# Kernel optimization log

Hardware: AMD Instinct MI355X
Metric: run time of the kernel (lower is better)

The kernel has to match this reference:

```python
import jax, jax.numpy as jnp
import numpy as np

N = 100000
E = 1600000
D_IN = 256
HID = 128
EPS = 1e-5


def setup_inputs() -> dict:
    key = jax.random.key(0)
    ks = jax.random.split(key, 8)
    x = jax.random.normal(ks[0], (N, D_IN), dtype=jnp.float32)
    edge_index = jax.random.randint(ks[1], (2, E), 0, N, dtype=jnp.int64)
    edge_weight = jax.random.uniform(ks[2], (E,), dtype=jnp.float32)
    # GCNConv lin weights (glorot-ish scale) + bias
    W1 = jax.random.normal(ks[3], (D_IN, HID), dtype=jnp.float32) / np.sqrt(D_IN)
    b1 = jnp.zeros((HID,), dtype=jnp.float32)
    W2 = jax.random.normal(ks[4], (HID, HID), dtype=jnp.float32) / np.sqrt(HID)
    b2 = jnp.zeros((HID,), dtype=jnp.float32)
    # BatchNorm affine params
    g1 = jnp.ones((HID,), dtype=jnp.float32)
    be1 = jnp.zeros((HID,), dtype=jnp.float32)
    g2 = jnp.ones((HID,), dtype=jnp.float32)
    be2 = jnp.zeros((HID,), dtype=jnp.float32)
    return {"x": x, "edge_index": edge_index, "edge_weight": edge_weight,
            "W1": W1, "b1": b1, "g1": g1, "be1": be1,
            "W2": W2, "b2": b2, "g2": g2, "be2": be2}


def _gcn_layer(h, src, dst, w, W, b):
    # GCNConv(add_self_loops=False, normalize=False):
    # h' = h @ W; out[i] = sum_{(j->i)} w_ji * h'[j]; out += b
    h = h @ W                                   # [N, out_dim]
    msg = w[:, None] * jnp.take(h, src, axis=0)  # [E, out_dim]
    agg = jax.ops.segment_sum(msg, dst, num_segments=N)
    return agg + b


def _bn(h, gamma, beta):
    # BatchNorm1d with batch statistics (biased variance), training-mode math
    mean = jnp.mean(h, axis=0)
    var = jnp.mean(jnp.square(h - mean), axis=0)
    return (h - mean) * jax.lax.rsqrt(var + EPS) * gamma + beta


def reference(x, edge_index, edge_weight, W1, b1, g1, be1, W2, b2, g2, be2):
    src = edge_index[0]
    dst = edge_index[1]
    h = _gcn_layer(x, src, dst, edge_weight, W1, b1)
    h = jax.nn.relu(_bn(h, g1, be1))
    h = _gcn_layer(h, src, dst, edge_weight, W2, b2)
    h = jax.nn.relu(_bn(h, g2, be2))  # last_activation=True
    return h
```

## Files before the change

kernel.cpp:

```cpp
#include <hip/hip_runtime.h>
#include <hip/hip_bf16.h>

#define NNODES 100000
#define DIN    256
#define NHID   128
#define EPS    1e-5f
#define SHIFT  9
#define NB2    ((NNODES + 511) >> SHIFT)
#define BCAP2  9216
#define CURPAD 16
#define PH     2048

typedef __attribute__((ext_vector_type(8))) short short8v;
typedef __attribute__((ext_vector_type(4))) float f32x4;

static __device__ __forceinline__ unsigned short f2bf(float v) {
    __hip_bfloat16 b = __float2bfloat16(v);
    return *reinterpret_cast<unsigned short*>(&b);
}
static __device__ __forceinline__ float bfhi2f(unsigned int u) {
    union { unsigned int i; float f; } x; x.i = u & 0xFFFF0000u; return x.f;
}
static __device__ __forceinline__ float bflo2f(unsigned int u) {
    union { unsigned int i; float f; } x; x.i = u << 16; return x.f;
}

__global__ __launch_bounds__(256) void wtrans2_kernel(const float* __restrict__ W1,
                                                      const float* __restrict__ W2,
                                                      unsigned short* __restrict__ Wt1,
                                                      unsigned short* __restrict__ Wt2) {
    int i = blockIdx.x * 256 + threadIdx.x;
    if (i < DIN * NHID) {
        const int k = i >> 7, c = i & 127;
        Wt1[c * DIN + k] = f2bf(W1[i]);
    } else {
        i -= DIN * NHID;
        if (i < NHID * NHID) {
            const int k = i >> 7, c = i & 127;
            Wt2[c * NHID + k] = f2bf(W2[i]);
        }
    }
}

template <int K, int MODE>
__global__ __launch_bounds__(256) void mfma_gemm(const float* __restrict__ Af,
                                                 const unsigned short* __restrict__ Wtb,
                                                 const float* __restrict__ SS,
                                                 unsigned short* __restrict__ C, int M) {
    __shared__ float ssl[256];
    const int t = threadIdx.x;
    if (MODE == 1) {
        if (t < 256) ssl[t] = SS[t];
        __syncthreads();
    }

    const int wid = t >> 6;
    const int lane = t & 63;
    const int wr = wid >> 1, wc = wid & 1;
    const int l15 = lane & 15, g = lane >> 4;
    const int R0 = blockIdx.x * 128 + wr * 64;

    f32x4 acc[4][4] = {};

    for (int s = 0; s < K / 32; ++s) {
        short8v b[4];
#pragma unroll
        for (int n = 0; n < 4; ++n) {
            const int col = wc * 64 + n * 16 + l15;
            b[n] = *reinterpret_cast<const short8v*>(&Wtb[(size_t)col * K + s * 32 + g * 8]);
        }
        float sc[8], sh[8];
        if (MODE == 1) {
#pragma unroll
            for (int j = 0; j < 8; ++j) {
                sc[j] = ssl[s * 32 + g * 8 + j];
                sh[j] = ssl[128 + s * 32 + g * 8 + j];
            }
        }
        short8v a[4];
#pragma unroll
        for (int m = 0; m < 4; ++m) {
            int row = R0 + m * 16 + l15;
            row = row < M ? row : M - 1;
            const float* p = Af + (size_t)row * K + s * 32 + g * 8;
            const float4 v0 = *reinterpret_cast<const float4*>(p);
            const float4 v1 = *reinterpret_cast<const float4*>(p + 4);
            float vv[8] = {v0.x, v0.y, v0.z, v0.w, v1.x, v1.y, v1.z, v1.w};
            short8v av;
#pragma unroll
            for (int j = 0; j < 8; ++j) {
                float y = vv[j];
                if (MODE == 1) y = fmaxf(fmaf(y, sc[j], sh[j]), 0.f);
                av[j] = (short)f2bf(y);
            }
            a[m] = av;
        }
#pragma unroll
        for (int m = 0; m < 4; ++m)
#pragma unroll
            for (int n = 0; n < 4; ++n)
                acc[m][n] = __builtin_amdgcn_mfma_f32_16x16x32_bf16(a[m], b[n], acc[m][n], 0, 0, 0);
    }

#pragma unroll
    for (int m = 0; m < 4; ++m) {
#pragma unroll
        for (int q = 0; q < 4; ++q) {
            const int row = R0 + m * 16 + g * 4 + q;
            if (row < M) {
                unsigned short* cp = C + (size_t)row * NHID + wc * 64 + l15;
#pragma unroll
                for (int n = 0; n < 4; ++n)
                    cp[n * 16] = f2bf(acc[m][n][q]);
            }
        }
    }
}

__global__ __launch_bounds__(256) void part_kernel(const int* __restrict__ src,
                                                   const int* __restrict__ dst,
                                                   const float* __restrict__ w,
                                                   int* __restrict__ gcur,
                                                   int2* __restrict__ bstage, int E) {
    __shared__ int2 staged[PH];
    __shared__ unsigned char aux[PH];
    __shared__ int hist[NB2], scn[NB2], cur[NB2], gbase[NB2];
    __shared__ int part[256];

    const int t = threadIdx.x;
    const int nchunk = (E + PH - 1) / PH;
    for (int c = blockIdx.x; c < nchunk; c += gridDim.x) {
        const int e0 = c * PH;
        const int cnt = min(PH, E - e0);
        for (int i = t; i < NB2; i += 256) hist[i] = 0;
        __syncthreads();

        int2 pay[8];
        int bk[8];
#pragma unroll
        for (int j = 0; j < 8; ++j) {
            const int i = j * 256 + t;
            bk[j] = -1;
            if (i < cnt) {
                const int e = e0 + i;
                const int d = dst[e];
                bk[j] = d >> SHIFT;
                pay[j].x = src[e] | ((d & 511) << 17);
                pay[j].y = __float_as_int(w[e]);
                atomicAdd(&hist[bk[j]], 1);
            }
        }
        __syncthreads();

        part[t] = (t < NB2) ? hist[t] : 0;
        __syncthreads();
        for (int off = 1; off < 256; off <<= 1) {
            const int v = (t >= off) ? part[t - off] : 0;
            __syncthreads();
            part[t] += v;
            __syncthreads();
        }
        if (t < NB2) {
            const int ex = part[t] - hist[t];
            scn[t] = ex;
            cur[t] = ex;
        }
        __syncthreads();

#pragma unroll
        for (int j = 0; j < 8; ++j) {
            if (bk[j] >= 0) {
                const int p = atomicAdd(&cur[bk[j]], 1);
                staged[p] = pay[j];
                aux[p] = (unsigned char)bk[j];
            }
        }
        if (t < NB2 && hist[t] > 0) gbase[t] = atomicAdd(&gcur[t * CURPAD], hist[t]);
        __syncthreads();

        for (int i = t; i < cnt; i += 256) {
            const int b = aux[i];
            const int p = gbase[b] + (i - scn[b]);
            if (p < BCAP2) bstage[(size_t)b * BCAP2 + p] = staged[i];
        }
        __syncthreads();
    }
}

__global__ __launch_bounds__(256) void csr_kernel(const int* __restrict__ gcur,
                                                  const int2* __restrict__ bstage,
                                                  int2* __restrict__ row_be,
                                                  int2* __restrict__ s_iw) {
    const int b = blockIdx.x;
    const int t = threadIdx.x;
    int cnt = gcur[b * CURPAD];
    if (cnt > BCAP2) cnt = BCAP2;
    const int sbase = b * BCAP2;

    __shared__ int hist[512], cur[512];
    __shared__ int part[256];
    for (int i = t; i < 512; i += 256) hist[i] = 0;
    __syncthreads();
    for (int i = t; i < cnt; i += 256)
        atomicAdd(&hist[(bstage[sbase + i].x >> 17) & 511], 1);
    __syncthreads();

    int loc[2];
    loc[0] = hist[t * 2];
    loc[1] = hist[t * 2 + 1];
    const int s0 = loc[0] + loc[1];
    part[t] = s0;
    __syncthreads();
    for (int off = 1; off < 256; off <<= 1) {
        const int v = (t >= off) ? part[t - off] : 0;
        __syncthreads();
        part[t] += v;
        __syncthreads();
    }
    int run = part[t] - s0;
#pragma unroll
    for (int j = 0; j < 2; ++j) {
        const int lb = t * 2 + j;
        cur[lb] = run;
        const int d = (b << SHIFT) + lb;
        if (d < NNODES) {
            int2 be;
            be.x = sbase + run;
            be.y = sbase + run + loc[j];
            row_be[d] = be;
        }
        run += loc[j];
    }
    __syncthreads();

    for (int i = t; i < cnt; i += 256) {
        const int2 e = bstage[sbase + i];
        const int l = (e.x >> 17) & 511;
        const int p = atomicAdd(&cur[l], 1);
        int2 o;
        o.x = e.x & 0x1FFFF;
        o.y = e.y;
        s_iw[sbase + p] = o;
    }
}

__global__ __launch_bounds__(256) void aggregate_kernel(const unsigned short* __restrict__ hb,
                                                        const int2* __restrict__ row_be,
                                                        const int2* __restrict__ s_iw,
                                                        float* __restrict__ out, int n) {
    const int wid = (blockIdx.x * 256 + threadIdx.x) >> 6;
    if (wid >= n) return;
    const int lane = threadIdx.x & 63;
    const int grp = lane >> 4;
    const int l16 = lane & 15;
    const int2 be = row_be[wid];
    const int end = be.y;

    float acc[8] = {};
    int j = be.x + grp;
    for (; j + 4 < end; j += 8) {
        const int2 e0 = s_iw[j];
        const int2 e1 = s_iw[j + 4];
        const uint4 v0 = *reinterpret_cast<const uint4*>(hb + (size_t)e0.x * NHID + l16 * 8);
        const uint4 v1 = *reinterpret_cast<const uint4*>(hb + (size_t)e1.x * NHID + l16 * 8);
        const float w0 = __int_as_float(e0.y);
        const float w1 = __int_as_float(e1.y);
        acc[0] = fmaf(w0, bflo2f(v0.x), acc[0]); acc[1] = fmaf(w0, bfhi2f(v0.x), acc[1]);
        acc[2] = fmaf(w0, bflo2f(v0.y), acc[2]); acc[3] = fmaf(w0, bfhi2f(v0.y), acc[3]);
        acc[4] = fmaf(w0, bflo2f(v0.z), acc[4]); acc[5] = fmaf(w0, bfhi2f(v0.z), acc[5]);
        acc[6] = fmaf(w0, bflo2f(v0.w), acc[6]); acc[7] = fmaf(w0, bfhi2f(v0.w), acc[7]);
        acc[0] = fmaf(w1, bflo2f(v1.x), acc[0]); acc[1] = fmaf(w1, bfhi2f(v1.x), acc[1]);
        acc[2] = fmaf(w1, bflo2f(v1.y), acc[2]); acc[3] = fmaf(w1, bfhi2f(v1.y), acc[3]);
        acc[4] = fmaf(w1, bflo2f(v1.z), acc[4]); acc[5] = fmaf(w1, bfhi2f(v1.z), acc[5]);
        acc[6] = fmaf(w1, bflo2f(v1.w), acc[6]); acc[7] = fmaf(w1, bfhi2f(v1.w), acc[7]);
    }
    if (j < end) {
        const int2 e0 = s_iw[j];
        const uint4 v0 = *reinterpret_cast<const uint4*>(hb + (size_t)e0.x * NHID + l16 * 8);
        const float w0 = __int_as_float(e0.y);
        acc[0] = fmaf(w0, bflo2f(v0.x), acc[0]); acc[1] = fmaf(w0, bfhi2f(v0.x), acc[1]);
        acc[2] = fmaf(w0, bflo2f(v0.y), acc[2]); acc[3] = fmaf(w0, bfhi2f(v0.y), acc[3]);
        acc[4] = fmaf(w0, bflo2f(v0.z), acc[4]); acc[5] = fmaf(w0, bfhi2f(v0.z), acc[5]);
        acc[6] = fmaf(w0, bflo2f(v0.w), acc[6]); acc[7] = fmaf(w0, bfhi2f(v0.w), acc[7]);
    }
#pragma unroll
    for (int k = 0; k < 8; ++k) {
        acc[k] += __shfl_xor(acc[k], 16, 64);
        acc[k] += __shfl_xor(acc[k], 32, 64);
    }
    if (grp == 0) {
        float4 a, b;
        a.x = acc[0]; a.y = acc[1]; a.z = acc[2]; a.w = acc[3];
        b.x = acc[4]; b.y = acc[5]; b.z = acc[6]; b.w = acc[7];
        float4* op = reinterpret_cast<float4*>(out + (size_t)wid * NHID + l16 * 8);
        op[0] = a;
        op[1] = b;
    }
}

__global__ __launch_bounds__(256) void stats_kernel(const float* __restrict__ h,
                                                    float* __restrict__ sums, int nrows) {
    const int col = threadIdx.x & 127;
    const int half = threadIdx.x >> 7;
    float s = 0.f, sq = 0.f;
    for (int r = blockIdx.x * 2 + half; r < nrows; r += gridDim.x * 2) {
        const float v = h[(size_t)r * NHID + col];
        s += v;
        sq += v * v;
    }
    __shared__ float ls[256], lq[256];
    ls[threadIdx.x] = s;
    lq[threadIdx.x] = sq;
    __syncthreads();
    if (threadIdx.x < 128) {
        atomicAdd(&sums[col], ls[threadIdx.x] + ls[threadIdx.x + 128]);
        atomicAdd(&sums[128 + col], lq[threadIdx.x] + lq[threadIdx.x + 128]);
    }
}

__global__ void finalize_kernel(const float* __restrict__ sums,
                                const float* __restrict__ gamma,
                                const float* __restrict__ beta,
                                float* __restrict__ ss) {
    const int c = threadIdx.x;
    const float invN = 1.0f / (float)NNODES;
    const float mean = sums[c] * invN;
    const float var = sums[128 + c] * invN - mean * mean;
    const float scale = gamma[c] * rsqrtf(var + EPS);
    ss[c] = scale;
    ss[128 + c] = beta[c] - mean * scale;
}

__global__ __launch_bounds__(256) void apply_f32_kernel(const float* __restrict__ in,
                                                        const float* __restrict__ ss,
                                                        float* __restrict__ out, int n4) {
    const int idx = blockIdx.x * 256 + threadIdx.x;
    if (idx >= n4) return;
    const int c = (idx & 31) * 4;
    const float4 v = reinterpret_cast<const float4*>(in)[idx];
    const float4 sc = *reinterpret_cast<const float4*>(ss + c);
    const float4 sh = *reinterpret_cast<const float4*>(ss + 128 + c);
    float4 r;
    r.x = fmaxf(fmaf(v.x, sc.x, sh.x), 0.f);
    r.y = fmaxf(fmaf(v.y, sc.y, sh.y), 0.f);
    r.z = fmaxf(fmaf(v.z, sc.z, sh.z), 0.f);
    r.w = fmaxf(fmaf(v.w, sc.w, sh.w), 0.f);
    reinterpret_cast<float4*>(out)[idx] = r;
}

extern "C" void kernel_launch(void* const* d_in, const int* in_sizes, int n_in,
                              void* d_out, int out_size, void* d_ws, size_t ws_size,
                              hipStream_t stream) {
    const float* x   = (const float*)d_in[0];
    const int*   ei  = (const int*)d_in[1];
    const float* ew  = (const float*)d_in[2];
    const float* W1  = (const float*)d_in[3];
    const float* g1  = (const float*)d_in[5];
    const float* be1 = (const float*)d_in[6];
    const float* W2  = (const float*)d_in[7];
    const float* g2  = (const float*)d_in[9];
    const float* be2 = (const float*)d_in[10];
    float* out = (float*)d_out;

    const int M = NNODES;
    const int E = in_sizes[2];
    const int* src = ei;
    const int* dst = ei + E;

    unsigned short* hb = (unsigned short*)d_ws;
    float* agg   = (float*)(hb + (size_t)M * NHID);
    int2* bstage = (int2*)(agg + (size_t)M * NHID);
    int2* s_iw   = bstage + (size_t)NB2 * BCAP2;
    int2* row_be = s_iw + (size_t)NB2 * BCAP2;
    int* gcur    = (int*)(row_be + NNODES);
    unsigned short* Wt1b = (unsigned short*)(gcur + NB2 * CURPAD);
    unsigned short* Wt2b = Wt1b + DIN * NHID;
    float* sums  = (float*)(Wt2b + NHID * NHID);
    float* ss    = sums + 512;

    const int gemm_grid = (M + 127) / 128;
    const int n4 = M * NHID / 4;
    const int app_grid = (n4 + 255) / 256;
    const int agg_grid = (M * 64 + 255) / 256;
    const int part_grid = (E + PH - 1) / PH;

    wtrans2_kernel<<<(DIN * NHID + NHID * NHID + 255) / 256, 256, 0, stream>>>(W1, W2, Wt1b, Wt2b);
    hipMemsetAsync(gcur, 0, (size_t)NB2 * CURPAD * sizeof(int), stream);
    hipMemsetAsync(sums, 0, 512 * sizeof(float), stream);
    part_kernel<<<part_grid, 256, 0, stream>>>(src, dst, ew, gcur, bstage, E);
    csr_kernel<<<NB2, 256, 0, stream>>>(gcur, bstage, row_be, s_iw);

    mfma_gemm<DIN, 0><<<gemm_grid, 256, 0, stream>>>(x, Wt1b, nullptr, hb, M);
    aggregate_kernel<<<agg_grid, 256, 0, stream>>>(hb, row_be, s_iw, agg, M);
    stats_kernel<<<1024, 256, 0, stream>>>(agg, sums, M);
    finalize_kernel<<<1, 128, 0, stream>>>(sums, g1, be1, ss);

    mfma_gemm<NHID, 1><<<gemm_grid, 256, 0, stream>>>(agg, Wt2b, ss, hb, M);
    aggregate_kernel<<<agg_grid, 256, 0, stream>>>(hb, row_be, s_iw, agg, M);
    stats_kernel<<<1024, 256, 0, stream>>>(agg, sums + 256, M);
    finalize_kernel<<<1, 128, 0, stream>>>(sums + 256, g2, be2, ss);
    apply_f32_kernel<<<app_grid, 256, 0, stream>>>(agg, ss, out, n4);
}
```

Before: 363.0 us.

## Stage A tile in LDS with double buffering in MFMA GEMM

The GEMM now has the block cooperatively load each 128x32 A slice once from global memory. Each slice is converted to bf16, with the BN affine and ReLU applied in mode 1, and written into a padded, double-buffered LDS tile. Previously the two column-half wavefronts each loaded and converted the same A rows redundantly from global. The change halves global A traffic and conversion work and overlaps the next slice's load with the current MFMAs. In exchange it adds LDS usage and a barrier per K-step.

```diff
diff --git a/kernel.cpp b/kernel.cpp
--- a/kernel.cpp
+++ b/kernel.cpp
@@ -47,10 +47,14 @@
                                                  const unsigned short* __restrict__ Wtb,
                                                  const float* __restrict__ SS,
                                                  unsigned short* __restrict__ C, int M) {
+    constexpr int NS = K / 32;
+    constexpr int PADB = 40;
+    __shared__ unsigned short As[2][128 * PADB];
     __shared__ float ssl[256];
+
     const int t = threadIdx.x;
     if (MODE == 1) {
-        if (t < 256) ssl[t] = SS[t];
+        ssl[t] = SS[t];
         __syncthreads();
     }
 
@@ -58,55 +62,65 @@
     const int lane = t & 63;
     const int wr = wid >> 1, wc = wid & 1;
     const int l15 = lane & 15, g = lane >> 4;
-    const int R0 = blockIdx.x * 128 + wr * 64;
+    const int R0 = blockIdx.x * 128;
+    const int RW = R0 + wr * 64;
+
+    const int srow = t >> 3;
+    const int scol = (t & 7) * 4;
 
     f32x4 acc[4][4] = {};
 
-    for (int s = 0; s < K / 32; ++s) {
+    auto STAGE = [&](int s, int buf) {
+        const int k0 = s * 32;
+#pragma unroll
+        for (int i = 0; i < 4; ++i) {
+            const int row = srow + i * 32;
+            int grow = R0 + row;
+            grow = grow < M ? grow : M - 1;
+            float4 v = *reinterpret_cast<const float4*>(Af + (size_t)grow * K + k0 + scol);
+            if (MODE == 1) {
+                v.x = fmaxf(fmaf(v.x, ssl[k0 + scol],     ssl[128 + k0 + scol]),     0.f);
+                v.y = fmaxf(fmaf(v.y, ssl[k0 + scol + 1], ssl[128 + k0 + scol + 1]), 0.f);
+                v.z = fmaxf(fmaf(v.z, ssl[k0 + scol + 2], ssl[128 + k0 + scol + 2]), 0.f);
+                v.w = fmaxf(fmaf(v.w, ssl[k0 + scol + 3], ssl[128 + k0 + scol + 3]), 0.f);
+            }
+            ushort4 bv;
+            bv.x = f2bf(v.x); bv.y = f2bf(v.y); bv.z = f2bf(v.z); bv.w = f2bf(v.w);
+            *reinterpret_cast<ushort4*>(&As[buf][row * PADB + scol]) = bv;
+        }
+    };
+
+    STAGE(0, 0);
+    __syncthreads();
+
+    for (int s = 0; s < NS; ++s) {
+        if (s + 1 < NS) STAGE(s + 1, (s + 1) & 1);
+        const unsigned short* ab = As[s & 1];
         short8v b[4];
 #pragma unroll
         for (int n = 0; n < 4; ++n) {
             const int col = wc * 64 + n * 16 + l15;
             b[n] = *reinterpret_cast<const short8v*>(&Wtb[(size_t)col * K + s * 32 + g * 8]);
         }
-        float sc[8], sh[8];
-        if (MODE == 1) {
-#pragma unroll
-            for (int j = 0; j < 8; ++j) {
-                sc[j] = ssl[s * 32 + g * 8 + j];
-                sh[j] = ssl[128 + s * 32 + g * 8 + j];
-            }
-        }
         short8v a[4];
 #pragma unroll
         for (int m = 0; m < 4; ++m) {
-            int row = R0 + m * 16 + l15;
-            row = row < M ? row : M - 1;
-            const float* p = Af + (size_t)row * K + s * 32 + g * 8;
-            const float4 v0 = *reinterpret_cast<const float4*>(p);
-            const float4 v1 = *reinterpret_cast<const float4*>(p + 4);
-            float vv[8] = {v0.x, v0.y, v0.z, v0.w, v1.x, v1.y, v1.z, v1.w};
-            short8v av;
-#pragma unroll
-            for (int j = 0; j < 8; ++j) {
-                float y = vv[j];
-                if (MODE == 1) y = fmaxf(fmaf(y, sc[j], sh[j]), 0.f);
-                av[j] = (short)f2bf(y);
-            }
-            a[m] = av;
+            const int row = wr * 64 + m * 16 + l15;
+            a[m] = *reinterpret_cast<const short8v*>(&ab[row * PADB + g * 8]);
         }
 #pragma unroll
         for (int m = 0; m < 4; ++m)
 #pragma unroll
             for (int n = 0; n < 4; ++n)
                 acc[m][n] = __builtin_amdgcn_mfma_f32_16x16x32_bf16(a[m], b[n], acc[m][n], 0, 0, 0);
+        __syncthreads();
     }
 
 #pragma unroll
     for (int m = 0; m < 4; ++m) {
 #pragma unroll
         for (int q = 0; q < 4; ++q) {
-            const int row = R0 + m * 16 + g * 4 + q;
+            const int row = RW + m * 16 + g * 4 + q;
             if (row < M) {
                 unsigned short* cp = C + (size_t)row * NHID + wc * 64 + l15;
 #pragma unroll
```

After: 344.7 us. 1.05x faster.
